# Kernel tuning notes

Measured on AMD Instinct MI355X. Metric: run time of the kernel, lower is better.

The kernel has to match this reference:

```python
import jax, jax.numpy as jnp
import numpy as np

PC_RANGE = (-51.2, -51.2, -5.0, 51.2, 51.2, 3.0)
HEIGHTS = (0.0, 1.0, 2.0)
BEV_H, BEV_W = 320, 320
FEAT_H, FEAT_W = 128, 352
C, HID = 96, 64
MIN_DEPTH = 1e-3
BN_EPS = 1e-3


def _ref_points():
    # BEV cell centers at each sample height -> [n_h, N_cells, 3]
    x0, y0, _, x1, y1, _ = PC_RANGE
    xs = (jnp.arange(BEV_W, dtype=jnp.float32) + 0.5) / BEV_W * (x1 - x0) + x0
    ys = (jnp.arange(BEV_H, dtype=jnp.float32) + 0.5) / BEV_H * (y1 - y0) + y0
    yy, xx = jnp.meshgrid(ys, xs, indexing='ij')
    cells = jnp.stack([xx.ravel(), yy.ravel()], axis=-1)  # [N, 2]
    nh = len(HEIGHTS)
    N = cells.shape[0]
    h = jnp.asarray(HEIGHTS, jnp.float32)
    pts = jnp.concatenate([
        jnp.broadcast_to(cells[None], (nh, N, 2)),
        jnp.broadcast_to(h[:, None, None], (nh, N, 1)),
    ], axis=-1)
    return pts  # [nh, N, 3]


def _bilinear(feat, gx, gy):
    # grid_sample(mode=bilinear, padding=zeros, align_corners=True)
    # feat [C,H,W]; gx,gy [M] normalized to [-1,1] -> returns [M,C]
    H, W = feat.shape[1], feat.shape[2]
    x = (gx + 1.0) * 0.5 * (W - 1)
    y = (gy + 1.0) * 0.5 * (H - 1)
    x0 = jnp.floor(x)
    y0 = jnp.floor(y)
    wx = x - x0
    wy = y - y0

    def g(xi, yi):
        inb = ((xi >= 0) & (xi <= W - 1) & (yi >= 0) & (yi <= H - 1)).astype(feat.dtype)
        xc = jnp.clip(xi, 0, W - 1).astype(jnp.int32)
        yc = jnp.clip(yi, 0, H - 1).astype(jnp.int32)
        return feat[:, yc, xc] * inb  # [C, M]

    v = (g(x0, y0) * (1 - wx) * (1 - wy)
         + g(x0 + 1, y0) * wx * (1 - wy)
         + g(x0, y0 + 1) * (1 - wx) * wy
         + g(x0 + 1, y0 + 1) * wx * wy)
    return v.T  # [M, C]


def _lift_one(feat, M, he, dw1, db1, dw2, db2, sw1, sb1, sw2, sb2):
    pts = _ref_points()                       # [nh, N, 3]
    nh, N, _ = pts.shape
    hom = jnp.concatenate([pts, jnp.ones((nh, N, 1), pts.dtype)], axis=-1)
    proj = jnp.einsum('hnk,jk->hnj', hom, M)  # [nh, N, 4]
    depth = proj[..., 2]
    uv = proj[..., :2] / jnp.maximum(depth[..., None], 1e-5)
    gx = uv[..., 0] / (FEAT_W - 1) * 2.0 - 1.0
    gy = uv[..., 1] / (FEAT_H - 1) * 2.0 - 1.0
    valid = (depth > MIN_DEPTH) & (jnp.abs(gx) <= 1.0) & (jnp.abs(gy) <= 1.0)  # [nh, N]

    sampled = _bilinear(feat, gx.ravel(), gy.ravel()).reshape(nh, N, -1)
    sampled = sampled * valid[..., None].astype(sampled.dtype)
    sampled = sampled.transpose(1, 0, 2)      # [N, nh, C]
    valid_t = valid.T                          # [N, nh]

    d = jnp.log1p(jnp.maximum(depth, MIN_DEPTH)).T[..., None]  # [N, nh, 1]
    dfeat = jax.nn.relu(d @ dw1 + db1) @ dw2 + db2             # [N, nh, C]
    tokens = sampled + dfeat + he[None]

    logits = (jax.nn.relu(tokens @ sw1 + sb1) @ sw2 + sb2)[..., 0]  # [N, nh]
    logits = jnp.where(valid_t, logits, -jnp.inf)
    has_valid = valid_t.any(axis=1, keepdims=True)
    logits = jnp.where(has_valid, logits, 0.0)
    w = jax.nn.softmax(logits, axis=1)
    w = jnp.where(has_valid, w, 0.0)

    fused = jnp.einsum('nhc,nh->nc', sampled, w)  # [N, C]
    return fused.reshape(BEV_H, BEV_W, -1).transpose(2, 0, 1)  # [C, H, W]


def _conv_bn_relu(x, w, g, b, m, v):
    y = jax.lax.conv_general_dilated(x, w, (1, 1), ((1, 1), (1, 1)),
                                     dimension_numbers=('NCHW', 'OIHW', 'NCHW'))
    scale = (g / jnp.sqrt(v + BN_EPS))[None, :, None, None]
    y = (y - m[None, :, None, None]) * scale + b[None, :, None, None]
    return jax.nn.relu(y)


def setup_inputs() -> dict:
    key = jax.random.key(0)
    ks = jax.random.split(key, 12)
    B = 2
    image_feats = jax.random.normal(ks[0], (B, C, FEAT_H, FEAT_W), jnp.float32)
    fx = fy = 120.0
    cx, cy = FEAT_W / 2.0, FEAT_H / 2.0
    Mnp = np.array([[cx, -fx, 0.0, 0.0],
                    [cy, 0.0, -fy, 1.5 * fy],
                    [1.0, 0.0, 0.0, 0.0],
                    [0.0, 0.0, 0.0, 1.0]], np.float32)
    lidar2img = jnp.asarray(np.stack([Mnp] * B))
    return {
        'image_feats': image_feats,
        'lidar2img': lidar2img,
        'height_embedding': 0.02 * jax.random.normal(ks[1], (len(HEIGHTS), C), jnp.float32),
        'de_w1': jax.random.normal(ks[2], (1, HID), jnp.float32),
        'de_b1': jnp.zeros((HID,), jnp.float32),
        'de_w2': jax.random.normal(ks[3], (HID, C), jnp.float32) / np.sqrt(HID),
        'de_b2': jnp.zeros((C,), jnp.float32),
        'sh_w1': jax.random.normal(ks[4], (C, HID), jnp.float32) / np.sqrt(C),
        'sh_b1': jnp.zeros((HID,), jnp.float32),
        'sh_w2': jax.random.normal(ks[5], (HID, 1), jnp.float32) / np.sqrt(HID),
        'sh_b2': jnp.zeros((1,), jnp.float32),
        'conv1_w': jax.random.normal(ks[6], (C, C, 3, 3), jnp.float32) / np.sqrt(9 * C),
        'bn1_g': 1.0 + 0.1 * jax.random.normal(ks[7], (C,), jnp.float32),
        'bn1_b': 0.1 * jax.random.normal(ks[8], (C,), jnp.float32),
        'bn1_m': 0.1 * jax.random.normal(ks[9], (C,), jnp.float32),
        'bn1_v': jax.random.uniform(ks[10], (C,), jnp.float32, 0.5, 1.5),
        'conv2_w': jax.random.normal(ks[11], (C, C, 3, 3), jnp.float32) / np.sqrt(9 * C),
        'bn2_g': jnp.ones((C,), jnp.float32),
        'bn2_b': jnp.zeros((C,), jnp.float32),
        'bn2_m': jnp.zeros((C,), jnp.float32),
        'bn2_v': jnp.ones((C,), jnp.float32),
    }


def reference(image_feats, lidar2img, height_embedding,
              de_w1, de_b1, de_w2, de_b2, sh_w1, sh_b1, sh_w2, sh_b2,
              conv1_w, bn1_g, bn1_b, bn1_m, bn1_v,
              conv2_w, bn2_g, bn2_b, bn2_m, bn2_v):
    lift = lambda f, M: _lift_one(f, M, height_embedding,
                                  de_w1, de_b1, de_w2, de_b2,
                                  sh_w1, sh_b1, sh_w2, sh_b2)
    fused = jax.vmap(lift)(image_feats, lidar2img)  # [B, C, BEV_H, BEV_W]
    x = _conv_bn_relu(fused, conv1_w, bn1_g, bn1_b, bn1_m, bn1_v)
    x = _conv_bn_relu(x, conv2_w, bn2_g, bn2_b, bn2_m, bn2_v)
    return x
```

## Files before the change

### kernel.cpp

```cpp
#include <hip/hip_runtime.h>
#include <math.h>

typedef _Float16 f16x8 __attribute__((ext_vector_type(8)));
typedef _Float16 f16x4 __attribute__((ext_vector_type(4)));
typedef _Float16 f16x2 __attribute__((ext_vector_type(2)));
typedef float    f32x4 __attribute__((ext_vector_type(4)));

#define FEAT_H 128
#define FEAT_W 352
#define FPIX   (FEAT_H * FEAT_W)
#define BEV    320
#define NCELL  (BEV * BEV)
#define CH     96
#define PD     322
#define PPIX   (PD * PD)

#define N_PADF    (2 * PPIX * CH / 2)
#define OFF_BUFB  0
#define OFF_FS    0
#define OFF_FH    2883584
#define OFF_WT    (N_PADF)
#define OFF_HW    (OFF_WT + 82944)
#define OFF_BASE  (OFF_HW + 4096)
#define OFF_WD    (OFF_BASE + 192)
#define OFF_FLAG  (OFF_BASE + 256)
#define OFF_BUFA  (OFF_BASE + 512)

__global__ void k_setup(const float* __restrict__ dw2, const float* __restrict__ sw1,
                        const float* __restrict__ db2, const float* __restrict__ he,
                        const float* __restrict__ sb1, const float* __restrict__ db1,
                        const float* __restrict__ w1, const float* __restrict__ w2,
                        float* __restrict__ hW, float* __restrict__ baseT,
                        float* __restrict__ flagp,
                        _Float16* __restrict__ wt, _Float16* __restrict__ bufA) {
    const int bid = blockIdx.x;
    const int t = threadIdx.x;
    if (bid < 16) {
        const int idx = bid * 256 + t;
        const int j = idx >> 6, k = idx & 63;
        float s = 0.f;
        for (int c = 0; c < CH; c++) s = fmaf(dw2[j * CH + c], sw1[c * 64 + k], s);
        hW[idx] = s;
    } else if (bid == 16) {
        if (t < 192) {
            const int h = t >> 6, k = t & 63;
            float s = sb1[k];
            for (int c = 0; c < CH; c++) s = fmaf(db2[c] + he[h * CH + c], sw1[c * 64 + k], s);
            baseT[t] = s;
        } else if (t == 192) {
            float mx = 0.f;
            for (int j = 0; j < 64; j++) mx = fmaxf(mx, fabsf(db1[j]));
            flagp[0] = (mx == 0.f) ? 1.f : 0.f;
        }
    } else if (bid <= 664) {
        int idx = (bid - 17) * 256 + t;
        int cv = idx / 82944; int r = idx - cv * 82944;
        int tap = r / 9216;   int r2 = r - tap * 9216;
        int kc  = r2 / 3072;  int r3 = r2 - kc * 3072;
        int och = r3 / 1536;  int r4 = r3 - och * 1536;
        int ot  = r4 / 512;   int r5 = r4 - ot * 512;
        int l   = r5 >> 3;    int e  = r5 & 7;
        int oc  = och * 48 + ot * 16 + (l & 15);
        int ic  = kc * 32 + (l >> 4) * 8 + e;
        const float* src = cv ? w2 : w1;
        wt[idx] = (_Float16)src[(oc * 96 + ic) * 9 + tap];
    } else {
        int idx = (bid - 665) * 256 + t;
        if (idx >= 2568) return;
        int img = idx / 1284; int p = idx - img * 1284;
        int row, col;
        if (p < 322)      { row = 0;           col = p; }
        else if (p < 644) { row = 321;         col = p - 322; }
        else if (p < 964) { row = p - 644 + 1; col = 0; }
        else              { row = p - 964 + 1; col = 321; }
        _Float16* q = bufA + ((size_t)(img * PD + row) * PD + col) * CH;
        f16x8 z = {};
        #pragma unroll
        for (int c8 = 0; c8 < 12; ++c8) *(f16x8*)(q + c8 * 8) = z;
    }
}

__global__ __launch_bounds__(64) void k_setup2(const float* __restrict__ dw1,
                                               const float* __restrict__ hW,
                                               float* __restrict__ wD) {
    const int t = threadIdx.x;
    float s = 0.f;
    for (int j = 0; j < 64; j++) {
        float w = dw1[j];
        if (w > 0.f) s = fmaf(w, hW[j * 64 + t], s);
    }
    wD[t] = s;
}

__global__ void k_border(_Float16* __restrict__ buf) {
    int idx = blockIdx.x * 256 + threadIdx.x;
    if (idx >= 2568) return;
    int img = idx / 1284; int p = idx - img * 1284;
    int row, col;
    if (p < 322)      { row = 0;           col = p; }
    else if (p < 644) { row = 321;         col = p - 322; }
    else if (p < 964) { row = p - 644 + 1; col = 0; }
    else              { row = p - 964 + 1; col = 321; }
    _Float16* q = buf + ((size_t)(img * PD + row) * PD + col) * CH;
    f16x8 z = {};
    #pragma unroll
    for (int c8 = 0; c8 < 12; ++c8) *(f16x8*)(q + c8 * 8) = z;
}

__global__ __launch_bounds__(64) void k_feats(const float* __restrict__ feat,
                                              const float* __restrict__ sw1,
                                              _Float16* __restrict__ featS,
                                              _Float16* __restrict__ featH) {
    const int t = threadIdx.x;
    const int pb = blockIdx.x * 64;
    const int b = blockIdx.y;
    const float* fp = feat + (size_t)b * CH * FPIX + pb + t;
    _Float16* opH = featH + ((size_t)b * FPIX + pb + t) * 96;

    float acc[64];
    #pragma unroll
    for (int k = 0; k < 64; k++) acc[k] = 0.f;

    #pragma unroll
    for (int c8 = 0; c8 < 12; c8++) {
        float x[8];
        #pragma unroll
        for (int e = 0; e < 8; e++) x[e] = fp[(size_t)(c8 * 8 + e) * FPIX];
        f16x8 v;
        #pragma unroll
        for (int e = 0; e < 8; e++) v[e] = (_Float16)x[e];
        *(f16x8*)(opH + c8 * 8) = v;
        #pragma unroll
        for (int e = 0; e < 8; e++) {
            const float4* wr = (const float4*)(sw1 + (c8 * 8 + e) * 64);
            #pragma unroll
            for (int k4 = 0; k4 < 16; k4++) {
                float4 w = wr[k4];
                acc[4 * k4 + 0] = fmaf(x[e], w.x, acc[4 * k4 + 0]);
                acc[4 * k4 + 1] = fmaf(x[e], w.y, acc[4 * k4 + 1]);
                acc[4 * k4 + 2] = fmaf(x[e], w.z, acc[4 * k4 + 2]);
                acc[4 * k4 + 3] = fmaf(x[e], w.w, acc[4 * k4 + 3]);
            }
        }
    }
    _Float16* opS = featS + ((size_t)b * FPIX + pb + t) * 64;
    #pragma unroll
    for (int k8 = 0; k8 < 8; k8++) {
        f16x8 v;
        #pragma unroll
        for (int e = 0; e < 8; e++) v[e] = (_Float16)acc[k8 * 8 + e];
        *(f16x8*)(opS + k8 * 8) = v;
    }
}

__global__ __launch_bounds__(256, 4) void k_lift(const _Float16* __restrict__ featS,
                                                 const _Float16* __restrict__ featH,
                                                 const float* __restrict__ l2i,
                                                 const float* __restrict__ dw1,
                                                 const float* __restrict__ db1,
                                                 const float* __restrict__ sw2,
                                                 const float* __restrict__ sb2,
                                                 const float* __restrict__ hW,
                                                 const float* __restrict__ baseT,
                                                 const float* __restrict__ wD,
                                                 const float* __restrict__ flagp,
                                                 _Float16* __restrict__ out) {
    const int tid = threadIdx.x;
    const int g = tid >> 4;
    const int r = tid & 15;
    const int b = blockIdx.y;
    const int cell = blockIdx.x * 16 + g;
    const int i = cell / BEV, j = cell % BEV;
    const float px = ((j + 0.5f) / 320.0f) * 102.4f - 51.2f;
    const float py = ((i + 0.5f) / 320.0f) * 102.4f - 51.2f;
    const float* M = l2i + b * 16;
    const float m00 = M[0], m01 = M[1], m02 = M[2], m03 = M[3];
    const float m10 = M[4], m11 = M[5], m12 = M[6], m13 = M[7];
    const float m20 = M[8], m21 = M[9], m22 = M[10], m23 = M[11];

    const _Float16* fSb = featS + (size_t)b * FPIX * 64;
    const _Float16* fHb = featH + (size_t)b * FPIX * 96;

    const f32x4 wdv = *(const f32x4*)(wD + r * 4);
    const f32x4 sv  = *(const f32x4*)(sw2 + r * 4);
    const float sb2v = sb2[0];
    const bool fast = (flagp[0] != 0.f);

    int   ti[3][4];
    float tw[3][4];
    float logit[3];

    #pragma unroll
    for (int h = 0; h < 3; h++) {
        logit[h] = -INFINITY;
        ti[h][0] = ti[h][1] = ti[h][2] = ti[h][3] = 0;
        tw[h][0] = tw[h][1] = tw[h][2] = tw[h][3] = 0.f;
        const float z = (float)h;
        const float p0 = m03 + m00 * px + m01 * py + m02 * z;
        const float p1 = m13 + m10 * px + m11 * py + m12 * z;
        const float dep = m23 + m20 * px + m21 * py + m22 * z;
        const float dv = fmaxf(dep, 1e-5f);
        const float u = p0 / dv, v = p1 / dv;
        const float gx = (u / 351.0f) * 2.0f - 1.0f;
        const float gy = (v / 127.0f) * 2.0f - 1.0f;
        const bool valid = (dep > 1e-3f) && (fabsf(gx) <= 1.0f) && (fabsf(gy) <= 1.0f);
        if (!valid) continue;

        float xs = (gx + 1.0f) * 0.5f * 351.0f;
        float ys = (gy + 1.0f) * 0.5f * 127.0f;
        float xf = floorf(xs), yf = floorf(ys);
        int x0 = (int)xf, y0 = (int)yf;
        float wx = xs - xf, wy = ys - yf;
        int x1 = (x0 < FEAT_W - 1) ? x0 + 1 : x0;
        int y1 = (y0 < FEAT_H - 1) ? y0 + 1 : y0;
        ti[h][0] = y0 * FEAT_W + x0;  ti[h][1] = y0 * FEAT_W + x1;
        ti[h][2] = y1 * FEAT_W + x0;  ti[h][3] = y1 * FEAT_W + x1;
        const float tw0 = (1.f - wx) * (1.f - wy), tw1 = wx * (1.f - wy);
        const float tw2 = (1.f - wx) * wy,         tw3 = wx * wy;
        tw[h][0] = tw0; tw[h][1] = tw1; tw[h][2] = tw2; tw[h][3] = tw3;

        const float dl = log1pf(fmaxf(dep, 1e-3f));

        f16x4 t0 = *(const f16x4*)(fSb + (size_t)ti[h][0] * 64 + r * 4);
        f16x4 t1 = *(const f16x4*)(fSb + (size_t)ti[h][1] * 64 + r * 4);
        f16x4 t2 = *(const f16x4*)(fSb + (size_t)ti[h][2] * 64 + r * 4);
        f16x4 t3 = *(const f16x4*)(fSb + (size_t)ti[h][3] * 64 + r * 4);
        const f32x4 bs = *(const f32x4*)(baseT + h * 64 + r * 4);

        float hid[4];
        if (fast) {
            #pragma unroll
            for (int k = 0; k < 4; k++) hid[k] = fmaf(dl, wdv[k], bs[k]);
        } else {
            #pragma unroll
            for (int k = 0; k < 4; k++) hid[k] = bs[k];
            for (int jj = 0; jj < 64; jj++) {
                float hd = fmaxf(fmaf(dl, dw1[jj], db1[jj]), 0.f);
                const f32x4 hv = *(const f32x4*)(hW + jj * 64 + r * 4);
                #pragma unroll
                for (int k = 0; k < 4; k++) hid[k] = fmaf(hd, hv[k], hid[k]);
            }
        }
        float part = 0.f;
        #pragma unroll
        for (int k = 0; k < 4; k++) {
            float s = fmaf(tw0, (float)t0[k], fmaf(tw1, (float)t1[k],
                      fmaf(tw2, (float)t2[k], tw3 * (float)t3[k])));
            part = fmaf(fmaxf(hid[k] + s, 0.f), sv[k], part);
        }
        #pragma unroll
        for (int m = 1; m < 16; m <<= 1) part += __shfl_xor(part, m, 16);
        logit[h] = part + sb2v;
    }

    const float mx = fmaxf(logit[0], fmaxf(logit[1], logit[2]));
    float wh[3] = {0.f, 0.f, 0.f};
    if (mx > -INFINITY) {
        float e0 = (logit[0] > -INFINITY) ? expf(logit[0] - mx) : 0.f;
        float e1 = (logit[1] > -INFINITY) ? expf(logit[1] - mx) : 0.f;
        float e2 = (logit[2] > -INFINITY) ? expf(logit[2] - mx) : 0.f;
        const float inv = 1.0f / (e0 + e1 + e2);
        wh[0] = e0 * inv; wh[1] = e1 * inv; wh[2] = e2 * inv;
    }

    float acc4[4] = {0.f, 0.f, 0.f, 0.f};
    float acc2[2] = {0.f, 0.f};
    #pragma unroll
    for (int h = 0; h < 3; h++) {
        if (wh[h] > 0.f) {
            #pragma unroll
            for (int t = 0; t < 4; t++) {
                const float c = wh[h] * tw[h][t];
                const _Float16* gp = fHb + (size_t)ti[h][t] * 96;
                f16x4 v4 = *(const f16x4*)(gp + r * 4);
                f16x2 v2 = *(const f16x2*)(gp + 64 + r * 2);
                #pragma unroll
                for (int k = 0; k < 4; k++) acc4[k] = fmaf(c, (float)v4[k], acc4[k]);
                acc2[0] = fmaf(c, (float)v2[0], acc2[0]);
                acc2[1] = fmaf(c, (float)v2[1], acc2[1]);
            }
        }
    }
    _Float16* op = out + ((size_t)(b * PD + i + 1) * PD + (j + 1)) * CH;
    f16x4 s4;
    #pragma unroll
    for (int k = 0; k < 4; k++) s4[k] = (_Float16)acc4[k];
    *(f16x4*)(op + r * 4) = s4;
    f16x2 s2;
    s2[0] = (_Float16)acc2[0];
    s2[1] = (_Float16)acc2[1];
    *(f16x2*)(op + 64 + r * 2) = s2;
}

#define LOAD_FRAGS(WF, PF, STEP) do {                                              \
    constexpr int _tap = (STEP) / 3, _kc = (STEP) % 3;                             \
    constexpr int _r = _tap / 3, _s = _tap % 3;                                    \
    _Pragma("unroll")                                                              \
    for (int ot = 0; ot < 3; ++ot)                                                 \
        WF[ot] = *(const f16x8*)(wtb + _tap * 9216 + _kc * 3072 + ot * 512);       \
    _Pragma("unroll")                                                              \
    for (int pt = 0; pt < 4; ++pt)                                                 \
        PF[pt] = *(const f16x8*)(&sA[((2 * rp + (pt >> 1) + _r) * 34               \
                         + (pt & 1) * 16 + _s + n) * 104 + _kc * 32 + q * 8]);     \
} while (0)

#define DO_MFMA(WF, PF) do {                                                       \
    _Pragma("unroll")                                                              \
    for (int ot = 0; ot < 3; ++ot)                                                 \
        _Pragma("unroll")                                                          \
        for (int pt = 0; pt < 4; ++pt)                                             \
            acc[ot][pt] = __builtin_amdgcn_mfma_f32_16x16x32_f16(                  \
                              WF[ot], PF[pt], acc[ot][pt], 0, 0, 0);               \
} while (0)

#define SAB(S) LOAD_FRAGS(wfb, pfb, (S) + 1); DO_MFMA(wfa, pfa);
#define SBA(S) LOAD_FRAGS(wfa, pfa, (S) + 1); DO_MFMA(wfb, pfb);

template<int MODE>
__global__ __launch_bounds__(512, 4) void k_conv_mfma(
        const _Float16* __restrict__ in, const _Float16* __restrict__ wt,
        const float* __restrict__ bng, const float* __restrict__ bnb,
        const float* __restrict__ bnm, const float* __restrict__ bnv,
        void* __restrict__ outv) {
    __shared__ _Float16 sA[10 * 34 * 104];
    const int tid = threadIdx.x;
    const int w = tid >> 6, lane = tid & 63, q = lane >> 4, n = lane & 15;
    const int rp = w >> 1;
    const int och = w & 1;

    const int bid = blockIdx.x;
    const int swz = (bid & 7) * 100 + (bid >> 3);
    const int b = swz / 400;
    const int r2 = swz - b * 400;
    const int ty = r2 / 10, tx = r2 - ty * 10;
    const int x0 = tx * 32, y0 = ty * 8;

    const _Float16* inb = in + (size_t)b * PPIX * CH;

    for (int idx = tid; idx < 10 * 34 * 12; idx += 512) {
        int pix = idx / 12, c8 = idx - pix * 12;
        int rr = pix / 34, cc = pix - rr * 34;
        *(f16x8*)(&sA[pix * 104 + c8 * 8]) =
            *(const f16x8*)(inb + ((size_t)(y0 + rr) * PD + (x0 + cc)) * CH + c8 * 8);
    }
    __syncthreads();

    f32x4 acc[3][4];
    #pragma unroll
    for (int ot = 0; ot < 3; ot++)
        #pragma unroll
        for (int pt = 0; pt < 4; pt++) acc[ot][pt] = (f32x4){0.f, 0.f, 0.f, 0.f};

    const _Float16* wtb = wt + och * 1536 + lane * 8;

    f16x8 wfa[3], wfb[3], pfa[4], pfb[4];
    LOAD_FRAGS(wfa, pfa, 0);
    SAB(0)  SBA(1)  SAB(2)  SBA(3)  SAB(4)  SBA(5)  SAB(6)  SBA(7)
    SAB(8)  SBA(9)  SAB(10) SBA(11) SAB(12) SBA(13) SAB(14) SBA(15)
    SAB(16) SBA(17) SAB(18) SBA(19) SAB(20) SBA(21) SAB(22) SBA(23)
    SAB(24) SBA(25)
    DO_MFMA(wfa, pfa);

    float scv[3][4], shv[3][4];
    #pragma unroll
    for (int ot = 0; ot < 3; ot++)
        #pragma unroll
        for (int rg = 0; rg < 4; rg++) {
            int oc = och * 48 + ot * 16 + q * 4 + rg;
            scv[ot][rg] = bng[oc] * rsqrtf(bnv[oc] + 1e-3f);
            shv[ot][rg] = fmaf(-bnm[oc], scv[ot][rg], bnb[oc]);
        }

    if (MODE == 0) {
        _Float16* outb = (_Float16*)outv + (size_t)b * PPIX * CH;
        #pragma unroll
        for (int pt = 0; pt < 4; pt++) {
            const int orow = y0 + 2 * rp + (pt >> 1) + 1;
            const int ocol = x0 + (pt & 1) * 16 + n + 1;
            _Float16* op = outb + ((size_t)orow * PD + ocol) * CH + och * 48 + q * 4;
            #pragma unroll
            for (int ot = 0; ot < 3; ot++) {
                f16x4 pv;
                #pragma unroll
                for (int rg = 0; rg < 4; rg++)
                    pv[rg] = (_Float16)fmaxf(fmaf(acc[ot][pt][rg], scv[ot][rg], shv[ot][rg]), 0.f);
                *(f16x4*)(op + ot * 16) = pv;
            }
        }
    } else {
        float* outb = (float*)outv + (size_t)b * CH * NCELL;
        #pragma unroll
        for (int pt = 0; pt < 4; pt++) {
            const int prow = y0 + 2 * rp + (pt >> 1);
            const int pcol = x0 + (pt & 1) * 16 + n;
            #pragma unroll
            for (int ot = 0; ot < 3; ot++)
                #pragma unroll
                for (int rg = 0; rg < 4; rg++) {
                    int oc = och * 48 + ot * 16 + q * 4 + rg;
                    outb[(size_t)oc * NCELL + prow * BEV + pcol] =
                        fmaxf(fmaf(acc[ot][pt][rg], scv[ot][rg], shv[ot][rg]), 0.f);
                }
        }
    }
}

extern "C" void kernel_launch(void* const* d_in, const int* in_sizes, int n_in,
                              void* d_out, int out_size, void* d_ws, size_t ws_size,
                              hipStream_t stream) {
    const float* feat = (const float*)d_in[0];
    const float* l2i  = (const float*)d_in[1];
    const float* he   = (const float*)d_in[2];
    const float* dw1  = (const float*)d_in[3];
    const float* db1  = (const float*)d_in[4];
    const float* dw2  = (const float*)d_in[5];
    const float* db2  = (const float*)d_in[6];
    const float* sw1  = (const float*)d_in[7];
    const float* sb1  = (const float*)d_in[8];
    const float* sw2  = (const float*)d_in[9];
    const float* sb2  = (const float*)d_in[10];
    const float* c1w  = (const float*)d_in[11];
    const float* bn1g = (const float*)d_in[12];
    const float* bn1b = (const float*)d_in[13];
    const float* bn1m = (const float*)d_in[14];
    const float* bn1v = (const float*)d_in[15];
    const float* c2w  = (const float*)d_in[16];
    const float* bn2g = (const float*)d_in[17];
    const float* bn2b = (const float*)d_in[18];
    const float* bn2m = (const float*)d_in[19];
    const float* bn2v = (const float*)d_in[20];

    float* ws = (float*)d_ws;
    _Float16*  bufB   = (_Float16*)(ws + OFF_BUFB);
    _Float16*  featS  = (_Float16*)(ws + OFF_FS);
    _Float16*  featH  = (_Float16*)(ws + OFF_FH);
    _Float16*  wtp    = (_Float16*)(ws + OFF_WT);
    float*     hW     = ws + OFF_HW;
    float*     baseT  = ws + OFF_BASE;
    float*     wD     = ws + OFF_WD;
    float*     flagp  = ws + OFF_FLAG;
    _Float16*  bufA   = (_Float16*)(ws + OFF_BUFA);
    _Float16*  wt1    = wtp;
    _Float16*  wt2    = wtp + 82944;

    hipLaunchKernelGGL(k_setup, dim3(676), dim3(256), 0, stream,
                       dw2, sw1, db2, he, sb1, db1, c1w, c2w,
                       hW, baseT, flagp, wtp, bufA);
    hipLaunchKernelGGL(k_setup2, dim3(1), dim3(64), 0, stream, dw1, hW, wD);
    hipLaunchKernelGGL(k_feats, dim3(FPIX / 64, 2), dim3(64), 0, stream,
                       feat, sw1, featS, featH);
    hipLaunchKernelGGL(k_lift, dim3(NCELL / 16, 2), dim3(256), 0, stream,
                       featS, featH, l2i, dw1, db1, sw2, sb2, hW, baseT, wD, flagp, bufA);
    hipLaunchKernelGGL(k_border, dim3(11), dim3(256), 0, stream, bufB);
    hipLaunchKernelGGL((k_conv_mfma<0>), dim3(800), dim3(512), 0, stream,
                       bufA, wt1, bn1g, bn1b, bn1m, bn1v, (void*)bufB);
    hipLaunchKernelGGL((k_conv_mfma<1>), dim3(800), dim3(512), 0, stream,
                       bufB, wt2, bn2g, bn2b, bn2m, bn2v, d_out);
}
```

Measured before the change: 332.8 us.

## Split feature projection into transpose kernel and MFMA matmul kernel

The fused per-pixel kernel that converted features to fp16 and computed a 96x64 projection with scalar FMAs is split in two. One kernel only transposes and casts features, using 256-thread blocks where each thread handles 24 channels. A second kernel runs the projection as 16x16x32 fp16 MFMAs, with the sw1 weights pre-packed into fp16 fragment layout during setup. This removes the heavy scalar FMA loop and its 64-register accumulator, at the cost of an extra launch, a reread of featH, fp16 rounding of the inputs before the matmul, and scattered 2-byte stores.

```diff
diff --git a/kernel.cpp b/kernel.cpp
--- a/kernel.cpp
+++ b/kernel.cpp
@@ -24,14 +24,15 @@
 #define OFF_BASE  (OFF_HW + 4096)
 #define OFF_WD    (OFF_BASE + 192)
 #define OFF_FLAG  (OFF_BASE + 256)
-#define OFF_BUFA  (OFF_BASE + 512)
+#define OFF_SW1H  (OFF_BASE + 512)
+#define OFF_BUFA  (OFF_SW1H + 3072)
 
 __global__ void k_setup(const float* __restrict__ dw2, const float* __restrict__ sw1,
                         const float* __restrict__ db2, const float* __restrict__ he,
                         const float* __restrict__ sb1, const float* __restrict__ db1,
                         const float* __restrict__ w1, const float* __restrict__ w2,
                         float* __restrict__ hW, float* __restrict__ baseT,
-                        float* __restrict__ flagp,
+                        float* __restrict__ flagp, _Float16* __restrict__ sw1p,
                         _Float16* __restrict__ wt, _Float16* __restrict__ bufA) {
     const int bid = blockIdx.x;
     const int t = threadIdx.x;
@@ -52,8 +53,16 @@
             for (int j = 0; j < 64; j++) mx = fmaxf(mx, fabsf(db1[j]));
             flagp[0] = (mx == 0.f) ? 1.f : 0.f;
         }
-    } else if (bid <= 664) {
-        int idx = (bid - 17) * 256 + t;
+    } else if (bid <= 40) {
+        const int idx = (bid - 17) * 256 + t;
+        const int e  = idx & 7;
+        const int l  = (idx >> 3) & 63;
+        const int nt = (idx >> 9) & 3;
+        const int kc = idx >> 11;
+        const int q = l >> 4, n = l & 15;
+        sw1p[idx] = (_Float16)sw1[(kc * 32 + q * 8 + e) * 64 + nt * 16 + n];
+    } else if (bid <= 688) {
+        int idx = (bid - 41) * 256 + t;
         int cv = idx / 82944; int r = idx - cv * 82944;
         int tap = r / 9216;   int r2 = r - tap * 9216;
         int kc  = r2 / 3072;  int r3 = r2 - kc * 3072;
@@ -65,7 +74,7 @@
         const float* src = cv ? w2 : w1;
         wt[idx] = (_Float16)src[(oc * 96 + ic) * 9 + tap];
     } else {
-        int idx = (bid - 665) * 256 + t;
+        int idx = (bid - 689) * 256 + t;
         if (idx >= 2568) return;
         int img = idx / 1284; int p = idx - img * 1284;
         int row, col;
@@ -107,50 +116,63 @@
     for (int c8 = 0; c8 < 12; ++c8) *(f16x8*)(q + c8 * 8) = z;
 }
 
-__global__ __launch_bounds__(64) void k_feats(const float* __restrict__ feat,
-                                              const float* __restrict__ sw1,
-                                              _Float16* __restrict__ featS,
-                                              _Float16* __restrict__ featH) {
-    const int t = threadIdx.x;
+__global__ __launch_bounds__(256) void k_tr(const float* __restrict__ feat,
+                                            _Float16* __restrict__ featH) {
+    const int tid = threadIdx.x;
+    const int kq = tid >> 6;
+    const int t = tid & 63;
     const int pb = blockIdx.x * 64;
     const int b = blockIdx.y;
-    const float* fp = feat + (size_t)b * CH * FPIX + pb + t;
-    _Float16* opH = featH + ((size_t)b * FPIX + pb + t) * 96;
-
-    float acc[64];
-    #pragma unroll
-    for (int k = 0; k < 64; k++) acc[k] = 0.f;
-
-    #pragma unroll
-    for (int c8 = 0; c8 < 12; c8++) {
-        float x[8];
-        #pragma unroll
-        for (int e = 0; e < 8; e++) x[e] = fp[(size_t)(c8 * 8 + e) * FPIX];
+    const float* fp = feat + (size_t)b * CH * FPIX + (size_t)(kq * 24) * FPIX + pb + t;
+    _Float16* opH = featH + ((size_t)b * FPIX + pb + t) * 96 + kq * 24;
+
+    float x[24];
+    #pragma unroll
+    for (int c = 0; c < 24; c++) x[c] = fp[(size_t)c * FPIX];
+    #pragma unroll
+    for (int c8 = 0; c8 < 3; c8++) {
         f16x8 v;
         #pragma unroll
-        for (int e = 0; e < 8; e++) v[e] = (_Float16)x[e];
+        for (int e = 0; e < 8; e++) v[e] = (_Float16)x[c8 * 8 + e];
         *(f16x8*)(opH + c8 * 8) = v;
-        #pragma unroll
-        for (int e = 0; e < 8; e++) {
-            const float4* wr = (const float4*)(sw1 + (c8 * 8 + e) * 64);
-            #pragma unroll
-            for (int k4 = 0; k4 < 16; k4++) {
-                float4 w = wr[k4];
-                acc[4 * k4 + 0] = fmaf(x[e], w.x, acc[4 * k4 + 0]);
-                acc[4 * k4 + 1] = fmaf(x[e], w.y, acc[4 * k4 + 1]);
-                acc[4 * k4 + 2] = fmaf(x[e], w.z, acc[4 * k4 + 2]);
-                acc[4 * k4 + 3] = fmaf(x[e], w.w, acc[4 * k4 + 3]);
-            }
-        }
-    }
-    _Float16* opS = featS + ((size_t)b * FPIX + pb + t) * 64;
-    #pragma unroll
-    for (int k8 = 0; k8 < 8; k8++) {
-        f16x8 v;
-        #pragma unroll
-        for (int e = 0; e < 8; e++) v[e] = (_Float16)acc[k8 * 8 + e];
-        *(f16x8*)(opS + k8 * 8) = v;
-    }
+    }
+}
+
+__global__ __launch_bounds__(512, 2) void k_fs(const _Float16* __restrict__ featH,
+                                               const _Float16* __restrict__ sw1p,
+                                               _Float16* __restrict__ featS) {
+    const int tid = threadIdx.x;
+    const int wid = tid >> 6, lane = tid & 63;
+    const int q = lane >> 4, n = lane & 15;
+    const int mt = blockIdx.x * 8 + wid;
+
+    f16x8 bf[3][4];
+    #pragma unroll
+    for (int kc = 0; kc < 3; kc++)
+        #pragma unroll
+        for (int nt = 0; nt < 4; nt++)
+            bf[kc][nt] = *(const f16x8*)(sw1p + ((kc * 4 + nt) * 64 + lane) * 8);
+
+    f16x8 a[3];
+    const _Float16* ar = featH + (size_t)(mt * 16 + n) * 96 + q * 8;
+    #pragma unroll
+    for (int kc = 0; kc < 3; kc++) a[kc] = *(const f16x8*)(ar + kc * 32);
+
+    f32x4 acc[4];
+    #pragma unroll
+    for (int nt = 0; nt < 4; nt++) acc[nt] = (f32x4){0.f, 0.f, 0.f, 0.f};
+    #pragma unroll
+    for (int kc = 0; kc < 3; kc++)
+        #pragma unroll
+        for (int nt = 0; nt < 4; nt++)
+            acc[nt] = __builtin_amdgcn_mfma_f32_16x16x32_f16(a[kc], bf[kc][nt], acc[nt], 0, 0, 0);
+
+    _Float16* os = featS + (size_t)(mt * 16 + q * 4) * 64 + n;
+    #pragma unroll
+    for (int nt = 0; nt < 4; nt++)
+        #pragma unroll
+        for (int rg = 0; rg < 4; rg++)
+            os[(size_t)rg * 64 + nt * 16] = (_Float16)acc[nt][rg];
 }
 
 __global__ __launch_bounds__(256, 4) void k_lift(const _Float16* __restrict__ featS,
@@ -439,16 +461,17 @@
     float*     baseT  = ws + OFF_BASE;
     float*     wD     = ws + OFF_WD;
     float*     flagp  = ws + OFF_FLAG;
+    _Float16*  sw1p   = (_Float16*)(ws + OFF_SW1H);
     _Float16*  bufA   = (_Float16*)(ws + OFF_BUFA);
     _Float16*  wt1    = wtp;
     _Float16*  wt2    = wtp + 82944;
 
-    hipLaunchKernelGGL(k_setup, dim3(676), dim3(256), 0, stream,
+    hipLaunchKernelGGL(k_setup, dim3(700), dim3(256), 0, stream,
                        dw2, sw1, db2, he, sb1, db1, c1w, c2w,
-                       hW, baseT, flagp, wtp, bufA);
+                       hW, baseT, flagp, sw1p, wtp, bufA);
     hipLaunchKernelGGL(k_setup2, dim3(1), dim3(64), 0, stream, dw1, hW, wD);
-    hipLaunchKernelGGL(k_feats, dim3(FPIX / 64, 2), dim3(64), 0, stream,
-                       feat, sw1, featS, featH);
+    hipLaunchKernelGGL(k_tr, dim3(FPIX / 64, 2), dim3(256), 0, stream, feat, featH);
+    hipLaunchKernelGGL(k_fs, dim3(704), dim3(512), 0, stream, featH, sw1p, featS);
     hipLaunchKernelGGL(k_lift, dim3(NCELL / 16, 2), dim3(256), 0, stream,
                        featS, featH, l2i, dw1, db1, sw2, sb2, hW, baseT, wD, flagp, bufA);
     hipLaunchKernelGGL(k_border, dim3(11), dim3(256), 0, stream, bufB);
```

Result: faster. 308.0 us (-7.4%).
